# Optimization experiments

Measured on AMD Instinct MI355X. Metric: run time of the kernel, lower is better.

Reference implementation:

```python
import jax, jax.numpy as jnp
import numpy as np

B, T, M = 64, 32, 64
IN_DIM, GNN, H, L = 256, 256, 4, 3
TEMP, OUT, NH, NLT = 256, 512, 8, 2
DIST_THR = 0.3


def _ln(x, s, b, eps=1e-5):
    mu = jnp.mean(x, -1, keepdims=True)
    v = jnp.mean(jnp.square(x - mu), -1, keepdims=True)
    return (x - mu) * jax.lax.rsqrt(v + eps) * s + b


def setup_inputs() -> dict:
    key = jax.random.key(0)
    ks = iter(jax.random.split(key, 64))
    def nrm(shape, scale=0.05):
        return jax.random.normal(next(ks), shape, jnp.float32) * scale
    C = GNN // H
    return dict(
        drone_feats=jax.random.normal(next(ks), (B, T, M, IN_DIM), jnp.float32),
        boxes=jax.random.uniform(next(ks), (B, T, M, 5), jnp.float32),
        drone_mask=jnp.ones((B, T, M), jnp.float32),
        in_proj_W=nrm((GNN, IN_DIM)), in_proj_b=jnp.zeros((GNN,), jnp.float32),
        gat_lin_W=nrm((L, GNN, GNN)), gat_edge_W=nrm((L, 3, GNN)),
        gat_att_src=nrm((L, H, C)), gat_att_dst=nrm((L, H, C)), gat_att_edge=nrm((L, H, C)),
        gat_bias=jnp.zeros((L, GNN), jnp.float32),
        gat_ln_s=jnp.ones((L, GNN), jnp.float32), gat_ln_b=jnp.zeros((L, GNN), jnp.float32),
        temp_W=nrm((TEMP, GNN)), temp_b=jnp.zeros((TEMP,), jnp.float32),
        pos_emb=nrm((1, T, TEMP), 0.02),
        qkv_W=nrm((NLT, 3 * TEMP, TEMP)), qkv_b=jnp.zeros((NLT, 3 * TEMP), jnp.float32),
        attn_out_W=nrm((NLT, TEMP, TEMP)), attn_out_b=jnp.zeros((NLT, TEMP), jnp.float32),
        ln1_s=jnp.ones((NLT, TEMP), jnp.float32), ln1_b=jnp.zeros((NLT, TEMP), jnp.float32),
        ln2_s=jnp.ones((NLT, TEMP), jnp.float32), ln2_b=jnp.zeros((NLT, TEMP), jnp.float32),
        ff1_W=nrm((NLT, 2 * TEMP, TEMP)), ff1_b=jnp.zeros((NLT, 2 * TEMP), jnp.float32),
        ff2_W=nrm((NLT, TEMP, 2 * TEMP)), ff2_b=jnp.zeros((NLT, TEMP), jnp.float32),
        pool_W=nrm((1, TEMP)), pool_b=jnp.zeros((1,), jnp.float32),
        out_W=nrm((OUT, TEMP)), out_b=jnp.zeros((OUT,), jnp.float32),
        out_ln_s=jnp.ones((OUT,), jnp.float32), out_ln_b=jnp.zeros((OUT,), jnp.float32),
    )


def reference(drone_feats, boxes, drone_mask, in_proj_W, in_proj_b, gat_lin_W, gat_edge_W,
              gat_att_src, gat_att_dst, gat_att_edge, gat_bias, gat_ln_s, gat_ln_b,
              temp_W, temp_b, pos_emb, qkv_W, qkv_b, attn_out_W, attn_out_b,
              ln1_s, ln1_b, ln2_s, ln2_b, ff1_W, ff1_b, ff2_W, ff2_b,
              pool_W, pool_b, out_W, out_b, out_ln_s, out_ln_b):
    Bv, Tv, Mv, _ = drone_feats.shape
    Hh, Cc = gat_att_src.shape[1], gat_att_src.shape[2]
    valid = drone_mask > 0.5                                  # [B,T,M]

    # ---- batched radius-graph build (dense masked form over tiny M) ----
    pos = boxes[..., 1:3]                                     # [B,T,M,2]
    rel = pos[..., None, :, :] - pos[..., :, None, :]         # [B,T,s,d,2] = pos_d - pos_s
    sq = jnp.sum(jnp.square(rel), -1)
    dist = jnp.sqrt(jnp.maximum(sq, 1e-12))                   # [B,T,s,d]
    eye = jnp.eye(Mv, dtype=bool)
    pair_valid = valid[..., :, None] & valid[..., None, :]
    adj = pair_valid & (dist < DIST_THR) & (~eye)             # real directed edges (s->d)
    eattr = jnp.where(adj[..., None], jnp.concatenate([dist[..., None], rel], -1), 0.0)
    # GATConv(add_self_loops=True, fill_value='mean'): self-loop attr = mean incoming attr
    deg = jnp.maximum(jnp.sum(adj, axis=-2), 1).astype(eattr.dtype)   # incoming per dst
    loop_attr = jnp.sum(eattr, axis=-3) / deg[..., None]              # [B,T,M,3]
    eattr = jnp.where(eye[:, :, None], loop_attr[..., None, :, :], eattr)
    full_adj = adj | (eye & pair_valid)

    # ---- spatial GAT stack ----
    x = jnp.einsum('btmi,gi->btmg', drone_feats, in_proj_W) + in_proj_b
    x = x * valid[..., None]
    for l in range(gat_lin_W.shape[0]):
        h = jnp.einsum('btmg,gk->btmk', x, gat_lin_W[l]).reshape(Bv, Tv, Mv, Hh, Cc)
        a_src = jnp.einsum('btmhc,hc->btmh', h, gat_att_src[l])
        a_dst = jnp.einsum('btmhc,hc->btmh', h, gat_att_dst[l])
        w_e = jnp.einsum('ehc,hc->eh', gat_edge_W[l].reshape(3, Hh, Cc), gat_att_edge[l])
        a_edge = jnp.einsum('btsde,eh->btsdh', eattr, w_e)
        logits = a_src[..., :, None, :] + a_dst[..., None, :, :] + a_edge
        logits = jnp.where(logits >= 0, logits, 0.2 * logits)        # LeakyReLU(0.2)
        logits = jnp.where(full_adj[..., None], logits, jnp.float32(-1e9))
        alpha = jax.nn.softmax(logits, axis=-3)                      # softmax over src per dst
        msg = jnp.einsum('btsdh,btshc->btdhc', alpha, h).reshape(Bv, Tv, Mv, Hh * Cc) + gat_bias[l]
        x = jax.nn.relu(_ln(msg + x, gat_ln_s[l], gat_ln_b[l]))

    nvalid = jnp.maximum(jnp.sum(valid, -1), 1).astype(x.dtype)
    frame = jnp.sum(x * valid[..., None], axis=-2) / nvalid[..., None]   # [B,T,GNN]

    # ---- temporal transformer (norm_first, relu, 2 layers) ----
    y = jnp.einsum('btg,dg->btd', frame, temp_W) + temp_b
    y = y + pos_emb[:, :Tv, :]
    D = y.shape[-1]
    hd = D // NH
    for l in range(qkv_W.shape[0]):
        z = _ln(y, ln1_s[l], ln1_b[l])
        qkv = z @ qkv_W[l].T + qkv_b[l]
        q, k, v = jnp.split(qkv, 3, axis=-1)
        q = q.reshape(Bv, Tv, NH, hd).transpose(0, 2, 1, 3)
        k = k.reshape(Bv, Tv, NH, hd).transpose(0, 2, 1, 3)
        v = v.reshape(Bv, Tv, NH, hd).transpose(0, 2, 1, 3)
        att = jax.nn.softmax(jnp.einsum('bhqd,bhkd->bhqk', q, k) / jnp.sqrt(jnp.float32(hd)), -1)
        o = jnp.einsum('bhqk,bhkd->bhqd', att, v).transpose(0, 2, 1, 3).reshape(Bv, Tv, D)
        y = y + o @ attn_out_W[l].T + attn_out_b[l]
        z = _ln(y, ln2_s[l], ln2_b[l])
        y = y + jax.nn.relu(z @ ff1_W[l].T + ff1_b[l]) @ ff2_W[l].T + ff2_b[l]

    wts = jax.nn.softmax(y @ pool_W.T + pool_b, axis=1)   # [B,T,1]
    pooled = jnp.sum(y * wts, axis=1)                     # [B,D]
    out = pooled @ out_W.T + out_b
    return jax.nn.relu(_ln(out, out_ln_s, out_ln_b))
```

## Files before the change

### kernel.cpp

```cpp
#include <hip/hip_runtime.h>
#include <math.h>

#define BT 2048

typedef __attribute__((ext_vector_type(8))) short bf16x8;
typedef __attribute__((ext_vector_type(4))) float f32x4;
typedef __attribute__((ext_vector_type(4))) unsigned short u16x4;

__device__ inline unsigned short f2bf(float f) {
    union { float f; unsigned u; } v; v.f = f;
    unsigned r = (v.u >> 16) & 1u;
    return (unsigned short)((v.u + 0x7FFFu + r) >> 16);
}
__device__ inline float bf2f(unsigned short s) {
    union { unsigned u; float f; } v; v.u = ((unsigned)s) << 16;
    return v.f;
}

__device__ inline float dot4(const float4 a, const float4 b) {
    return fmaf(a.x, b.x, fmaf(a.y, b.y, fmaf(a.z, b.z, a.w * b.w)));
}

union F8 { float4 v2[2]; float f[8]; };

#define XP 264

__global__ __launch_bounds__(256) void k_prep(const float* __restrict__ inW,
                                              const float* __restrict__ gatW,
                                              unsigned short* __restrict__ dst) {
    int gid = blockIdx.x * 256 + threadIdx.x;
    int mat = gid >> 14;
    int r   = gid & 16383;
    int ks  = r >> 10;
    int nt  = (r >> 6) & 15;
    int lane = r & 63;
    int ln15 = lane & 15, q = lane >> 4;
    int n  = nt * 16 + ln15;
    int k0 = ks * 32 + q * 8;
    const float* src; bool tr;
    if (mat == 0) { src = inW; tr = true; }
    else          { src = gatW + (size_t)(mat - 1) * 65536; tr = false; }
    unsigned short* d = dst + ((size_t)mat * 16384 + r) * 16;
    if (ks < 8) {
        #pragma unroll
        for (int j = 0; j < 8; j++) {
            float v = tr ? src[n * 256 + k0 + j] : src[(size_t)(k0 + j) * 256 + n];
            unsigned short hi = f2bf(v);
            d[j]     = hi;
            d[8 + j] = f2bf(v - bf2f(hi));
        }
    } else {
        #pragma unroll
        for (int j = 0; j < 8; j++) { d[j] = 0; d[8 + j] = 0; }
    }
}

__global__ __launch_bounds__(512, 2) void k_gnn(const float* __restrict__ feats,
                                                const float* __restrict__ boxes,
                                                const float* __restrict__ maskp,
                                                const unsigned short* __restrict__ BswAll,
                                                const float* __restrict__ inb,
                                                const float* __restrict__ edgeW,
                                                const float* __restrict__ attSg,
                                                const float* __restrict__ attDg,
                                                const float* __restrict__ attEg,
                                                const float* __restrict__ gbias,
                                                const float* __restrict__ glns,
                                                const float* __restrict__ glnb,
                                                float* __restrict__ framebuf) {
    int bt = blockIdx.x;
    size_t fbase = (size_t)bt * 64 * 256;

    __shared__ unsigned short xH[64 * XP];
    __shared__ unsigned short xL[64 * XP];
    __shared__ unsigned short hT[256 * 136];
    __shared__ float pxS[64], pyS[64], vmS[64];
    __shared__ float loopS[192];
    __shared__ float asrcS[8][64], adstS[8][64];
    __shared__ float wESall[36];
    __shared__ float sumsS[64][8];
    __shared__ float mrsS[64][2];
    __shared__ float nvS;

    int tid = threadIdx.x, lane = tid & 63, w = tid >> 6;
    int ln15 = lane & 15, q = lane >> 4;
    int nt0 = w * 2;
    int head = w >> 1;
    int base_d = (w & 1) * 32;

    unsigned short* fH = hT;
    unsigned short* fL = hT + 64 * XP;

    if (tid < 64) {
        const float* bx = boxes + (size_t)(bt * 64 + tid) * 5;
        pxS[tid] = bx[1];
        pyS[tid] = bx[2];
        vmS[tid] = maskp[bt * 64 + tid];
    } else if (tid < 100) {
        int idx = tid - 64;
        int l = idx / 12, r2 = idx - l * 12;
        int e = r2 >> 2, h2 = r2 & 3;
        float sm = 0.f;
        const float* ew = edgeW + (size_t)l * 768 + e * 256 + h2 * 64;
        const float* ae = attEg + (size_t)l * 256 + h2 * 64;
        for (int c = 0; c < 64; c++) sm += ew[c] * ae[c];
        wESall[idx] = sm;
    }
    #pragma unroll
    for (int j = 0; j < 8; j++) {
        int g = j * 2048 + tid * 4;
        int row = g >> 8, col = g & 255;
        float4 v4 = *(const float4*)&feats[fbase + g];
        union { u16x4 v; unsigned short u[4]; } H4, L4;
        float vf[4] = {v4.x, v4.y, v4.z, v4.w};
        #pragma unroll
        for (int jj = 0; jj < 4; jj++) {
            H4.u[jj] = f2bf(vf[jj]);
            L4.u[jj] = f2bf(vf[jj] - bf2f(H4.u[jj]));
        }
        *(u16x4*)&fH[row * XP + col] = H4.v;
        *(u16x4*)&fL[row * XP + col] = L4.v;
    }
    __syncthreads();

    {
        int d = tid >> 3, part = tid & 7;
        float pxd = pxS[d], pyd = pyS[d];
        bool vd = vmS[d] > 0.5f;
        float deg = 0.f, s0 = 0.f, s1 = 0.f, s2 = 0.f;
        #pragma unroll
        for (int k = 0; k < 8; k++) {
            int s = part * 8 + k;
            float rx = pxd - pxS[s], ry = pyd - pyS[s];
            float dist = sqrtf(fmaxf(rx * rx + ry * ry, 1e-12f));
            bool adj = vd && (vmS[s] > 0.5f) && (dist < 0.3f) && (s != d);
            if (adj) { deg += 1.f; s0 += dist; s1 += rx; s2 += ry; }
        }
        #pragma unroll
        for (int off = 1; off < 8; off <<= 1) {
            deg += __shfl_xor(deg, off);
            s0  += __shfl_xor(s0, off);
            s1  += __shfl_xor(s1, off);
            s2  += __shfl_xor(s2, off);
        }
        if (part == 0) {
            float dg = fmaxf(deg, 1.f);
            loopS[d * 3 + 0] = s0 / dg;
            loopS[d * 3 + 1] = s1 / dg;
            loopS[d * 3 + 2] = s2 / dg;
        }
    }
    if (tid == 0) {
        float nv = 0.f;
        for (int m = 0; m < 64; m++) nv += vmS[m] > 0.5f ? 1.f : 0.f;
        nvS = fmaxf(nv, 1.f);
    }

    {
        f32x4 acc[4][2];
        #pragma unroll
        for (int mt = 0; mt < 4; mt++)
            #pragma unroll
            for (int ntl = 0; ntl < 2; ntl++) acc[mt][ntl] = (f32x4){0.f, 0.f, 0.f, 0.f};
        for (int ks = 0; ks < 8; ks++) {
            bf16x8 bhi[2], blo[2];
            #pragma unroll
            for (int ntl = 0; ntl < 2; ntl++) {
                const unsigned short* fb = &BswAll[((size_t)(ks * 16 + nt0 + ntl) * 64 + lane) * 16];
                bhi[ntl] = *(const bf16x8*)&fb[0];
                blo[ntl] = *(const bf16x8*)&fb[8];
            }
            #pragma unroll
            for (int mt = 0; mt < 4; mt++) {
                int ao = (mt * 16 + ln15) * XP + ks * 32 + q * 8;
                bf16x8 ahi = *(const bf16x8*)&fH[ao];
                bf16x8 alo = *(const bf16x8*)&fL[ao];
                #pragma unroll
                for (int ntl = 0; ntl < 2; ntl++) {
                    acc[mt][ntl] = __builtin_amdgcn_mfma_f32_16x16x32_bf16(ahi, bhi[ntl], acc[mt][ntl], 0, 0, 0);
                    acc[mt][ntl] = __builtin_amdgcn_mfma_f32_16x16x32_bf16(alo, bhi[ntl], acc[mt][ntl], 0, 0, 0);
                    acc[mt][ntl] = __builtin_amdgcn_mfma_f32_16x16x32_bf16(ahi, blo[ntl], acc[mt][ntl], 0, 0, 0);
                }
            }
        }
        #pragma unroll
        for (int ntl = 0; ntl < 2; ntl++) {
            int c = (nt0 + ntl) * 16 + ln15;
            float bv = inb[c];
            #pragma unroll
            for (int mt = 0; mt < 4; mt++) {
                #pragma unroll
                for (int r = 0; r < 4; r++) {
                    int m = mt * 16 + q * 4 + r;
                    float v = (acc[mt][ntl][r] + bv) * (vmS[m] > 0.5f ? 1.f : 0.f);
                    unsigned short hi = f2bf(v);
                    xH[m * XP + c] = hi;
                    xL[m * XP + c] = f2bf(v - bf2f(hi));
                }
            }
        }
    }
    __syncthreads();

    for (int l = 0; l < 3; l++) {
        const unsigned short* BswL = BswAll + (size_t)(1 + l) * 16384 * 16;
        const float* attSl = attSg + (size_t)l * 256;
        const float* attDl = attDg + (size_t)l * 256;
        const float* biasl = gbias + (size_t)l * 256;
        const float* lnsl  = glns + (size_t)l * 256;
        const float* lnbl  = glnb + (size_t)l * 256;
        const float* wES   = wESall + l * 12;

        f32x4 acc[4][2];
        #pragma unroll
        for (int mt = 0; mt < 4; mt++)
            #pragma unroll
            for (int ntl = 0; ntl < 2; ntl++) acc[mt][ntl] = (f32x4){0.f, 0.f, 0.f, 0.f};
        for (int ks = 0; ks < 8; ks++) {
            bf16x8 bhi[2], blo[2];
            #pragma unroll
            for (int ntl = 0; ntl < 2; ntl++) {
                const unsigned short* fb = &BswL[((size_t)(ks * 16 + nt0 + ntl) * 64 + lane) * 16];
                bhi[ntl] = *(const bf16x8*)&fb[0];
                blo[ntl] = *(const bf16x8*)&fb[8];
            }
            #pragma unroll
            for (int mt = 0; mt < 4; mt++) {
                int ao = (mt * 16 + ln15) * XP + ks * 32 + q * 8;
                bf16x8 ahi = *(const bf16x8*)&xH[ao];
                bf16x8 alo = *(const bf16x8*)&xL[ao];
                #pragma unroll
                for (int ntl = 0; ntl < 2; ntl++) {
                    acc[mt][ntl] = __builtin_amdgcn_mfma_f32_16x16x32_bf16(ahi, bhi[ntl], acc[mt][ntl], 0, 0, 0);
                    acc[mt][ntl] = __builtin_amdgcn_mfma_f32_16x16x32_bf16(alo, bhi[ntl], acc[mt][ntl], 0, 0, 0);
                    acc[mt][ntl] = __builtin_amdgcn_mfma_f32_16x16x32_bf16(ahi, blo[ntl], acc[mt][ntl], 0, 0, 0);
                }
            }
        }

        {
            float pSrc[4][4], pDst[4][4];
            #pragma unroll
            for (int mt = 0; mt < 4; mt++)
                #pragma unroll
                for (int r = 0; r < 4; r++) { pSrc[mt][r] = 0.f; pDst[mt][r] = 0.f; }
            #pragma unroll
            for (int ntl = 0; ntl < 2; ntl++) {
                int c = (nt0 + ntl) * 16 + ln15;
                float aS = attSl[c], aD = attDl[c];
                #pragma unroll
                for (int mt = 0; mt < 4; mt++) {
                    #pragma unroll
                    for (int r = 0; r < 4; r++) {
                        float v = acc[mt][ntl][r];
                        pSrc[mt][r] = fmaf(v, aS, pSrc[mt][r]);
                        pDst[mt][r] = fmaf(v, aD, pDst[mt][r]);
                        unsigned short hi = f2bf(v);
                        unsigned short lo = f2bf(v - bf2f(hi));
                        int s = mt * 16 + q * 4 + r;
                        hT[c * 136 + s] = hi;
                        hT[c * 136 + 64 + s] = lo;
                    }
                }
            }
            #pragma unroll
            for (int off = 1; off < 16; off <<= 1) {
                #pragma unroll
                for (int mt = 0; mt < 4; mt++)
                    #pragma unroll
                    for (int r = 0; r < 4; r++) {
                        pSrc[mt][r] += __shfl_xor(pSrc[mt][r], off);
                        pDst[mt][r] += __shfl_xor(pDst[mt][r], off);
                    }
            }
            if (ln15 == 0) {
                #pragma unroll
                for (int mt = 0; mt < 4; mt++)
                    #pragma unroll
                    for (int r = 0; r < 4; r++) {
                        int m = mt * 16 + q * 4 + r;
                        asrcS[w][m] = pSrc[mt][r];
                        adstS[w][m] = pDst[mt][r];
                    }
            }
        }
        __syncthreads();

        f32x4 macc[2][4];
        #pragma unroll
        for (int t = 0; t < 2; t++)
            #pragma unroll
            for (int ct = 0; ct < 4; ct++) macc[t][ct] = (f32x4){0.f, 0.f, 0.f, 0.f};
        {
            float pxd[2], pyd[2], adstv[2], lp0[2], lp1[2], lp2[2];
            int dcur[2];
            bool vdv[2];
            #pragma unroll
            for (int t = 0; t < 2; t++) {
                int d = base_d + t * 16 + ln15;
                dcur[t] = d;
                pxd[t] = pxS[d]; pyd[t] = pyS[d];
                vdv[t] = vmS[d] > 0.5f;
                adstv[t] = adstS[2 * head][d] + adstS[2 * head + 1][d];
                lp0[t] = loopS[d * 3 + 0];
                lp1[t] = loopS[d * 3 + 1];
                lp2[t] = loopS[d * 3 + 2];
            }
            float we0 = wES[head], we1 = wES[4 + head], we2 = wES[8 + head];

            float lg[2][16];
            #pragma unroll
            for (int ks = 0; ks < 2; ks++) {
                int s0 = ks * 32 + q * 8;
                F8 PX, PY, VM, AS, A1;
                PX.v2[0] = *(const float4*)&pxS[s0]; PX.v2[1] = *(const float4*)&pxS[s0 + 4];
                PY.v2[0] = *(const float4*)&pyS[s0]; PY.v2[1] = *(const float4*)&pyS[s0 + 4];
                VM.v2[0] = *(const float4*)&vmS[s0]; VM.v2[1] = *(const float4*)&vmS[s0 + 4];
                AS.v2[0] = *(const float4*)&asrcS[2 * head][s0];
                AS.v2[1] = *(const float4*)&asrcS[2 * head][s0 + 4];
                A1.v2[0] = *(const float4*)&asrcS[2 * head + 1][s0];
                A1.v2[1] = *(const float4*)&asrcS[2 * head + 1][s0 + 4];
                #pragma unroll
                for (int j = 0; j < 8; j++) {
                    int s = s0 + j;
                    float vsf = VM.f[j];
                    float asv = AS.f[j] + A1.f[j];
                    #pragma unroll
                    for (int t = 0; t < 2; t++) {
                        float rx = pxd[t] - PX.f[j], ry = pyd[t] - PY.f[j];
                        float dist = sqrtf(fmaxf(rx * rx + ry * ry, 1e-12f));
                        bool self = (s == dcur[t]);
                        bool adj = vdv[t] && (vsf > 0.5f) && (dist < 0.3f) && !self;
                        float e0 = adj ? dist : (self ? lp0[t] : 0.f);
                        float e1 = adj ? rx   : (self ? lp1[t] : 0.f);
                        float e2 = adj ? ry   : (self ? lp2[t] : 0.f);
                        bool fa = adj || (self && vdv[t]);
                        float lv = asv + adstv[t] + e0 * we0 + e1 * we1 + e2 * we2;
                        lv = lv >= 0.f ? lv : 0.2f * lv;
                        lg[t][ks * 8 + j] = fa ? lv : -1e9f;
                    }
                }
            }

            bf16x8 ah[2][2], al[2][2];
            #pragma unroll
            for (int t = 0; t < 2; t++) {
                float mx = lg[t][0];
                #pragma unroll
                for (int j = 1; j < 16; j++) mx = fmaxf(mx, lg[t][j]);
                mx = fmaxf(mx, __shfl_xor(mx, 16));
                mx = fmaxf(mx, __shfl_xor(mx, 32));
                float ee[16], sm = 0.f;
                #pragma unroll
                for (int j = 0; j < 16; j++) { ee[j] = __expf(lg[t][j] - mx); sm += ee[j]; }
                sm += __shfl_xor(sm, 16);
                sm += __shfl_xor(sm, 32);
                float inv = 1.f / sm;
                #pragma unroll
                for (int ks2 = 0; ks2 < 2; ks2++) {
                    union { bf16x8 v; unsigned short u[8]; } H, L;
                    #pragma unroll
                    for (int j = 0; j < 8; j++) {
                        float a = ee[ks2 * 8 + j] * inv;
                        unsigned short hi = f2bf(a);
                        H.u[j] = hi;
                        L.u[j] = f2bf(a - bf2f(hi));
                    }
                    ah[t][ks2] = H.v; al[t][ks2] = L.v;
                }
            }

            #pragma unroll
            for (int t = 0; t < 2; t++) {
                #pragma unroll
                for (int ks2 = 0; ks2 < 2; ks2++) {
                    #pragma unroll
                    for (int ct = 0; ct < 4; ct++) {
                        const unsigned short* hb =
                            &hT[(size_t)(head * 64 + ct * 16 + ln15) * 136 + ks2 * 32 + q * 8];
                        bf16x8 bhi = *(const bf16x8*)&hb[0];
                        bf16x8 blo = *(const bf16x8*)&hb[64];
                        macc[t][ct] = __builtin_amdgcn_mfma_f32_16x16x32_bf16(ah[t][ks2], bhi, macc[t][ct], 0, 0, 0);
                        macc[t][ct] = __builtin_amdgcn_mfma_f32_16x16x32_bf16(al[t][ks2], bhi, macc[t][ct], 0, 0, 0);
                        macc[t][ct] = __builtin_amdgcn_mfma_f32_16x16x32_bf16(ah[t][ks2], blo, macc[t][ct], 0, 0, 0);
                    }
                }
            }
        }

        {
            float bsv[4], scv[4], bbv[4];
            #pragma unroll
            for (int ct = 0; ct < 4; ct++) {
                int c = head * 64 + ct * 16 + ln15;
                bsv[ct] = biasl[c];
                scv[ct] = lnsl[c];
                bbv[ct] = lnbl[c];
            }
            float xo[2][4][4];
            #pragma unroll
            for (int t = 0; t < 2; t++)
                #pragma unroll
                for (int r = 0; r < 4; r++) {
                    int d = base_d + t * 16 + q * 4 + r;
                    #pragma unroll
                    for (int ct = 0; ct < 4; ct++) {
                        int o = d * XP + head * 64 + ct * 16 + ln15;
                        xo[t][ct][r] = bf2f(xH[o]) + bf2f(xL[o]);
                    }
                }
            float ps[8], ps2[8];
            #pragma unroll
            for (int t = 0; t < 2; t++)
                #pragma unroll
                for (int r = 0; r < 4; r++) {
                    float s = 0.f, s2 = 0.f;
                    #pragma unroll
                    for (int ct = 0; ct < 4; ct++) {
                        float v = macc[t][ct][r] + xo[t][ct][r] + bsv[ct];
                        s += v; s2 += v * v;
                    }
                    ps[t * 4 + r] = s; ps2[t * 4 + r] = s2;
                }
            #pragma unroll
            for (int off = 1; off < 16; off <<= 1) {
                #pragma unroll
                for (int i = 0; i < 8; i++) {
                    ps[i]  += __shfl_xor(ps[i], off);
                    ps2[i] += __shfl_xor(ps2[i], off);
                }
            }
            if (ln15 == 0) {
                #pragma unroll
                for (int t = 0; t < 2; t++)
                    #pragma unroll
                    for (int r = 0; r < 4; r++) {
                        int d = base_d + t * 16 + q * 4 + r;
                        sumsS[d][head * 2 + 0] = ps[t * 4 + r];
                        sumsS[d][head * 2 + 1] = ps2[t * 4 + r];
                    }
            }
            __syncthreads();
            if (tid < 64) {
                float S  = sumsS[tid][0] + sumsS[tid][2] + sumsS[tid][4] + sumsS[tid][6];
                float S2 = sumsS[tid][1] + sumsS[tid][3] + sumsS[tid][5] + sumsS[tid][7];
                float mu = S * (1.f / 256.f);
                float var = S2 * (1.f / 256.f) - mu * mu;
                mrsS[tid][0] = mu;
                mrsS[tid][1] = rsqrtf(var + 1e-5f);
            }
            __syncthreads();
            #pragma unroll
            for (int t = 0; t < 2; t++)
                #pragma unroll
                for (int r = 0; r < 4; r++) {
                    int d = base_d + t * 16 + q * 4 + r;
                    float mu = mrsS[d][0], rs = mrsS[d][1];
                    #pragma unroll
                    for (int ct = 0; ct < 4; ct++) {
                        float v = (macc[t][ct][r] + xo[t][ct][r] + bsv[ct] - mu) * rs * scv[ct] + bbv[ct];
                        v = fmaxf(v, 0.f);
                        unsigned short hi = f2bf(v);
                        int o = d * XP + head * 64 + ct * 16 + ln15;
                        xH[o] = hi;
                        xL[o] = f2bf(v - bf2f(hi));
                    }
                }
        }
        __syncthreads();
    }

    if (tid < 256) {
        float s = 0.f;
        for (int m = 0; m < 64; m++) {
            float xv = bf2f(xH[m * XP + tid]) + bf2f(xL[m * XP + tid]);
            s += xv * (vmS[m] > 0.5f ? 1.f : 0.f);
        }
        framebuf[(size_t)bt * 256 + tid] = s / nvS;
    }
}

__global__ __launch_bounds__(256) void k_temp4(const float* __restrict__ framebuf,
                                               const float* __restrict__ tW,
                                               const float* __restrict__ tb,
                                               const float* __restrict__ pe,
                                               float* __restrict__ ybuf) {
    int b4 = blockIdx.x;
    int tid = threadIdx.x;
    __shared__ float frS[4][256];
    #pragma unroll
    for (int t = 0; t < 4; t++) frS[t][tid] = framebuf[(size_t)(b4 * 4 + t) * 256 + tid];
    __syncthreads();
    float acc[4];
    #pragma unroll
    for (int t = 0; t < 4; t++) acc[t] = tb[tid] + pe[((b4 * 4 + t) & 31) * 256 + tid];
    const float* wrow = tW + (size_t)tid * 256;
    for (int g = 0; g < 256; g += 4) {
        float4 wv = *(const float4*)&wrow[g];
        #pragma unroll
        for (int t = 0; t < 4; t++) acc[t] += dot4(*(const float4*)&frS[t][g], wv);
    }
    #pragma unroll
    for (int t = 0; t < 4; t++) ybuf[(size_t)(b4 * 4 + t) * 256 + tid] = acc[t];
}

__global__ __launch_bounds__(256) void k_ln_qkv4(const float* __restrict__ ybuf,
                                                 const float* __restrict__ ln_s,
                                                 const float* __restrict__ ln_b,
                                                 const float* __restrict__ qW,
                                                 const float* __restrict__ qb,
                                                 float* __restrict__ qkvbuf) {
    int b4 = blockIdx.x, tid = threadIdx.x;
    int lane = tid & 63, wv = tid >> 6;
    __shared__ float zS[4][256];
    {
        int bt = b4 * 4 + wv;
        float4 yv = *(const float4*)&ybuf[(size_t)bt * 256 + lane * 4];
        float s = yv.x + yv.y + yv.z + yv.w;
        float s2 = yv.x * yv.x + yv.y * yv.y + yv.z * yv.z + yv.w * yv.w;
        #pragma unroll
        for (int off = 1; off < 64; off <<= 1) { s += __shfl_xor(s, off); s2 += __shfl_xor(s2, off); }
        float mu = s * (1.f / 256.f);
        float var = s2 * (1.f / 256.f) - mu * mu;
        float rstd = rsqrtf(var + 1e-5f);
        float4 ls = *(const float4*)&ln_s[lane * 4];
        float4 lb = *(const float4*)&ln_b[lane * 4];
        float4 z;
        z.x = (yv.x - mu) * rstd * ls.x + lb.x;
        z.y = (yv.y - mu) * rstd * ls.y + lb.y;
        z.z = (yv.z - mu) * rstd * ls.z + lb.z;
        z.w = (yv.w - mu) * rstd * ls.w + lb.w;
        *(float4*)&zS[wv][lane * 4] = z;
    }
    __syncthreads();
    for (int r = 0; r < 3; r++) {
        int j = r * 256 + tid;
        float acc[4];
        float bv = qb[j];
        #pragma unroll
        for (int t = 0; t < 4; t++) acc[t] = bv;
        const float* wrow = qW + (size_t)j * 256;
        for (int i = 0; i < 256; i += 4) {
            float4 wv4 = *(const float4*)&wrow[i];
            #pragma unroll
            for (int t = 0; t < 4; t++) acc[t] += dot4(*(const float4*)&zS[t][i], wv4);
        }
        #pragma unroll
        for (int t = 0; t < 4; t++) qkvbuf[(size_t)(b4 * 4 + t) * 768 + j] = acc[t];
    }
}

__global__ __launch_bounds__(64) void k_attn(const float* __restrict__ qkvbuf,
                                             float* __restrict__ obuf) {
    int blk = blockIdx.x;
    int b = blk >> 3, h = blk & 7;
    int tid = threadIdx.x;
    __shared__ float Ks[32 * 32], Vs[32 * 32];
    for (int idx = tid; idx < 1024; idx += 64) {
        int tk = idx >> 5, c = idx & 31;
        size_t qbase = ((size_t)(b * 32 + tk)) * 768 + h * 32 + c;
        Ks[idx] = qkvbuf[qbase + 256];
        Vs[idx] = qkvbuf[qbase + 512];
    }
    __syncthreads();
    if (tid < 32) {
        int tq = tid;
        float qv[32];
        size_t qb0 = ((size_t)(b * 32 + tq)) * 768 + h * 32;
        #pragma unroll
        for (int c = 0; c < 32; c++) qv[c] = qkvbuf[qb0 + c];
        float scr[32];
        float mx = -1e30f;
        #pragma unroll
        for (int tk = 0; tk < 32; tk++) {
            float dd = 0.f;
            #pragma unroll
            for (int c = 0; c < 32; c++) dd = fmaf(qv[c], Ks[tk * 32 + c], dd);
            dd *= 0.17677669529663687f;
            scr[tk] = dd;
            mx = fmaxf(mx, dd);
        }
        float sm = 0.f;
        #pragma unroll
        for (int tk = 0; tk < 32; tk++) { scr[tk] = __expf(scr[tk] - mx); sm += scr[tk]; }
        float inv = 1.f / sm;
        float o[32];
        #pragma unroll
        for (int c = 0; c < 32; c++) o[c] = 0.f;
        #pragma unroll
        for (int tk = 0; tk < 32; tk++) {
            float a = scr[tk] * inv;
            #pragma unroll
            for (int c = 0; c < 32; c++) o[c] = fmaf(a, Vs[tk * 32 + c], o[c]);
        }
        size_t ob = ((size_t)(b * 32 + tq)) * 256 + h * 32;
        #pragma unroll
        for (int c = 0; c < 32; c++) obuf[ob + c] = o[c];
    }
}

__global__ __launch_bounds__(256) void k_attn_out4(const float* __restrict__ obuf,
                                                   const float* __restrict__ W,
                                                   const float* __restrict__ bvec,
                                                   float* __restrict__ ybuf) {
    int b4 = blockIdx.x, tid = threadIdx.x;
    int lane = tid & 63, wv = tid >> 6;
    __shared__ float oS[4][256];
    *(float4*)&oS[wv][lane * 4] = *(const float4*)&obuf[(size_t)(b4 * 4 + wv) * 256 + lane * 4];
    __syncthreads();
    float acc[4];
    float bv = bvec[tid];
    #pragma unroll
    for (int t = 0; t < 4; t++) acc[t] = bv;
    const float* wrow = W + (size_t)tid * 256;
    for (int i = 0; i < 256; i += 4) {
        float4 wv4 = *(const float4*)&wrow[i];
        #pragma unroll
        for (int t = 0; t < 4; t++) acc[t] += dot4(*(const float4*)&oS[t][i], wv4);
    }
    #pragma unroll
    for (int t = 0; t < 4; t++) ybuf[(size_t)(b4 * 4 + t) * 256 + tid] += acc[t];
}

__global__ __launch_bounds__(256) void k_ff4(float* __restrict__ ybuf,
                                             const float* __restrict__ ln_s,
                                             const float* __restrict__ ln_b,
                                             const float* __restrict__ W1,
                                             const float* __restrict__ b1,
                                             const float* __restrict__ W2,
                                             const float* __restrict__ b2) {
    int b4 = blockIdx.x, tid = threadIdx.x;
    int lane = tid & 63, wv = tid >> 6;
    __shared__ float zS[4][256];
    __shared__ float fS[4][512];
    {
        int bt = b4 * 4 + wv;
        float4 yv = *(const float4*)&ybuf[(size_t)bt * 256 + lane * 4];
        float s = yv.x + yv.y + yv.z + yv.w;
        float s2 = yv.x * yv.x + yv.y * yv.y + yv.z * yv.z + yv.w * yv.w;
        #pragma unroll
        for (int off = 1; off < 64; off <<= 1) { s += __shfl_xor(s, off); s2 += __shfl_xor(s2, off); }
        float mu = s * (1.f / 256.f);
        float var = s2 * (1.f / 256.f) - mu * mu;
        float rstd = rsqrtf(var + 1e-5f);
        float4 ls = *(const float4*)&ln_s[lane * 4];
        float4 lb = *(const float4*)&ln_b[lane * 4];
        float4 z;
        z.x = (yv.x - mu) * rstd * ls.x + lb.x;
        z.y = (yv.y - mu) * rstd * ls.y + lb.y;
        z.z = (yv.z - mu) * rstd * ls.z + lb.z;
        z.w = (yv.w - mu) * rstd * ls.w + lb.w;
        *(float4*)&zS[wv][lane * 4] = z;
    }
    __syncthreads();
    for (int r = 0; r < 2; r++) {
        int j = r * 256 + tid;
        float acc[4];
        float bv = b1[j];
        #pragma unroll
        for (int t = 0; t < 4; t++) acc[t] = bv;
        const float* wrow = W1 + (size_t)j * 256;
        for (int i = 0; i < 256; i += 4) {
            float4 wv4 = *(const float4*)&wrow[i];
            #pragma unroll
            for (int t = 0; t < 4; t++) acc[t] += dot4(*(const float4*)&zS[t][i], wv4);
        }
        #pragma unroll
        for (int t = 0; t < 4; t++) fS[t][j] = fmaxf(acc[t], 0.f);
    }
    __syncthreads();
    float acc[4];
    float bv = b2[tid];
    #pragma unroll
    for (int t = 0; t < 4; t++) acc[t] = bv;
    const float* wrow = W2 + (size_t)tid * 512;
    for (int jj = 0; jj < 512; jj += 4) {
        float4 wv4 = *(const float4*)&wrow[jj];
        #pragma unroll
        for (int t = 0; t < 4; t++) acc[t] += dot4(*(const float4*)&fS[t][jj], wv4);
    }
    #pragma unroll
    for (int t = 0; t < 4; t++) {
        size_t idx = (size_t)(b4 * 4 + t) * 256 + tid;
        ybuf[idx] = ybuf[idx] + acc[t];
    }
}

__global__ __launch_bounds__(256) void k_pool_out(const float* __restrict__ ybuf,
                                                  const float* __restrict__ pW,
                                                  const float* __restrict__ pb,
                                                  const float* __restrict__ oW,
                                                  const float* __restrict__ ob,
                                                  const float* __restrict__ lns,
                                                  const float* __restrict__ lnb,
                                                  float* __restrict__ dout) {
    int b = blockIdx.x, tid = threadIdx.x;
    __shared__ float redP[256];
    __shared__ float wS[32];
    __shared__ float pS[256];
    __shared__ float red[8];
    int tq = tid >> 3, part = tid & 7;
    float partial = 0.f;
    {
        const float* yrow = ybuf + ((size_t)(b * 32 + tq)) * 256 + part * 32;
        const float* pwp = pW + part * 32;
        #pragma unroll
        for (int j = 0; j < 32; j += 4) {
            float4 yv = *(const float4*)&yrow[j];
            float4 wv = *(const float4*)&pwp[j];
            partial += dot4(yv, wv);
        }
    }
    redP[tid] = partial;
    __syncthreads();
    if (tid < 32) {
        float s = pb[0];
        for (int p = 0; p < 8; p++) s += redP[tid * 8 + p];
        float mx = s;
        #pragma unroll
        for (int off = 16; off; off >>= 1) mx = fmaxf(mx, __shfl_xor(mx, off));
        float e = __expf(s - mx);
        float sm = e;
        #pragma unroll
        for (int off = 16; off; off >>= 1) sm += __shfl_xor(sm, off);
        wS[tid] = e / sm;
    }
    __syncthreads();
    float p = 0.f;
    for (int t = 0; t < 32; t++) p += ybuf[((size_t)(b * 32 + t)) * 256 + tid] * wS[t];
    pS[tid] = p;
    __syncthreads();
    float accs[2];
    for (int r = 0; r < 2; r++) {
        int j = r * 256 + tid;
        float acc = ob[j];
        const float* wrow = oW + (size_t)j * 256;
        for (int g = 0; g < 256; g += 4) {
            float4 pv = *(const float4*)&pS[g];
            float4 wv = *(const float4*)&wrow[g];
            acc += dot4(pv, wv);
        }
        accs[r] = acc;
    }
    float s = accs[0] + accs[1];
    float s2 = accs[0] * accs[0] + accs[1] * accs[1];
    #pragma unroll
    for (int off = 32; off; off >>= 1) {
        s += __shfl_xor(s, off);
        s2 += __shfl_xor(s2, off);
    }
    int wid = threadIdx.x >> 6;
    int lane = threadIdx.x & 63;
    if (lane == 0) { red[wid] = s; red[4 + wid] = s2; }
    __syncthreads();
    s = red[0] + red[1] + red[2] + red[3];
    s2 = red[4] + red[5] + red[6] + red[7];
    float mu = s * (1.f / 512.f);
    float var = s2 * (1.f / 512.f) - mu * mu;
    float rstd = rsqrtf(var + 1e-5f);
    dout[b * 512 + tid]       = fmaxf((accs[0] - mu) * rstd * lns[tid] + lnb[tid], 0.f);
    dout[b * 512 + tid + 256] = fmaxf((accs[1] - mu) * rstd * lns[tid + 256] + lnb[tid + 256], 0.f);
}

extern "C" void kernel_launch(void* const* d_in, const int* in_sizes, int n_in,
                              void* d_out, int out_size, void* d_ws, size_t ws_size,
                              hipStream_t stream) {
    const float* drone_feats = (const float*)d_in[0];
    const float* boxes       = (const float*)d_in[1];
    const float* drone_mask  = (const float*)d_in[2];
    const float* in_proj_W   = (const float*)d_in[3];
    const float* in_proj_b   = (const float*)d_in[4];
    const float* gat_lin_W   = (const float*)d_in[5];
    const float* gat_edge_W  = (const float*)d_in[6];
    const float* gat_att_src = (const float*)d_in[7];
    const float* gat_att_dst = (const float*)d_in[8];
    const float* gat_att_edge= (const float*)d_in[9];
    const float* gat_bias    = (const float*)d_in[10];
    const float* gat_ln_s    = (const float*)d_in[11];
    const float* gat_ln_b    = (const float*)d_in[12];
    const float* temp_W      = (const float*)d_in[13];
    const float* temp_b      = (const float*)d_in[14];
    const float* pos_emb     = (const float*)d_in[15];
    const float* qkv_W       = (const float*)d_in[16];
    const float* qkv_b       = (const float*)d_in[17];
    const float* attn_out_W  = (const float*)d_in[18];
    const float* attn_out_b  = (const float*)d_in[19];
    const float* ln1_s       = (const float*)d_in[20];
    const float* ln1_b       = (const float*)d_in[21];
    const float* ln2_s       = (const float*)d_in[22];
    const float* ln2_b       = (const float*)d_in[23];
    const float* ff1_W       = (const float*)d_in[24];
    const float* ff1_b       = (const float*)d_in[25];
    const float* ff2_W       = (const float*)d_in[26];
    const float* ff2_b       = (const float*)d_in[27];
    const float* pool_W      = (const float*)d_in[28];
    const float* pool_b      = (const float*)d_in[29];
    const float* out_W       = (const float*)d_in[30];
    const float* out_b       = (const float*)d_in[31];
    const float* out_ln_s    = (const float*)d_in[32];
    const float* out_ln_b    = (const float*)d_in[33];
    float* out = (float*)d_out;

    float* ws = (float*)d_ws;
    unsigned short* Bsw = (unsigned short*)ws;
    size_t off = (size_t)(4 * 16384 * 16) / 2;
    float* framebuf = ws + off; off += (size_t)BT * 256;
    float* ybuf   = ws + off; off += (size_t)BT * 256;
    float* qkvbuf = ws + off; off += (size_t)BT * 768;
    float* obuf   = ws + off; off += (size_t)BT * 256;

    k_prep<<<dim3(256), dim3(256), 0, stream>>>(in_proj_W, gat_lin_W, Bsw);
    k_gnn<<<dim3(BT), dim3(512), 0, stream>>>(drone_feats, boxes, drone_mask, Bsw,
        in_proj_b, gat_edge_W, gat_att_src, gat_att_dst, gat_att_edge,
        gat_bias, gat_ln_s, gat_ln_b, framebuf);
    k_temp4<<<dim3(BT / 4), dim3(256), 0, stream>>>(framebuf, temp_W, temp_b, pos_emb, ybuf);
    for (int l = 0; l < 2; l++) {
        k_ln_qkv4<<<dim3(BT / 4), dim3(256), 0, stream>>>(ybuf, ln1_s + l * 256, ln1_b + l * 256,
            qkv_W + (size_t)l * 768 * 256, qkv_b + l * 768, qkvbuf);
        k_attn<<<dim3(512), dim3(64), 0, stream>>>(qkvbuf, obuf);
        k_attn_out4<<<dim3(BT / 4), dim3(256), 0, stream>>>(obuf,
            attn_out_W + (size_t)l * 65536, attn_out_b + l * 256, ybuf);
        k_ff4<<<dim3(BT / 4), dim3(256), 0, stream>>>(ybuf, ln2_s + l * 256, ln2_b + l * 256,
            ff1_W + (size_t)l * 131072, ff1_b + l * 512,
            ff2_W + (size_t)l * 131072, ff2_b + l * 256);
    }
    k_pool_out<<<dim3(64), dim3(256), 0, stream>>>(ybuf, pool_W, pool_b, out_W, out_b,
                                                   out_ln_s, out_ln_b, out);
}
```

Baseline: 1.136 ms.

## Alias GNN shared buffers and preload residual into accumulators to raise occupancy

Merges the xH/xL and hT shared arrays into one union buffer, which adds barriers where the regions are reused. The residual plus bias is loaded into the attention accumulators before the aggregation MFMAs, so the separate xo register array goes away. The softmax/aggregation loop now handles one tile at a time to cut live registers, and launch bounds ask for 4 blocks per CU instead of 2. The aim is lower LDS and VGPR use for higher occupancy, at the cost of extra syncs and possible spills if the register budget is too tight.

```diff
diff --git a/kernel.cpp b/kernel.cpp
--- a/kernel.cpp
+++ b/kernel.cpp
@@ -55,7 +55,7 @@
     }
 }
 
-__global__ __launch_bounds__(512, 2) void k_gnn(const float* __restrict__ feats,
+__global__ __launch_bounds__(512, 4) void k_gnn(const float* __restrict__ feats,
                                                 const float* __restrict__ boxes,
                                                 const float* __restrict__ maskp,
                                                 const unsigned short* __restrict__ BswAll,
@@ -71,9 +71,7 @@
     int bt = blockIdx.x;
     size_t fbase = (size_t)bt * 64 * 256;
 
-    __shared__ unsigned short xH[64 * XP];
-    __shared__ unsigned short xL[64 * XP];
-    __shared__ unsigned short hT[256 * 136];
+    __shared__ unsigned short U[256 * 136];
     __shared__ float pxS[64], pyS[64], vmS[64];
     __shared__ float loopS[192];
     __shared__ float asrcS[8][64], adstS[8][64];
@@ -88,8 +86,8 @@
     int head = w >> 1;
     int base_d = (w & 1) * 32;
 
-    unsigned short* fH = hT;
-    unsigned short* fL = hT + 64 * XP;
+    unsigned short* xH = U;
+    unsigned short* xL = U + 64 * XP;
 
     if (tid < 64) {
         const float* bx = boxes + (size_t)(bt * 64 + tid) * 5;
@@ -118,8 +116,8 @@
             H4.u[jj] = f2bf(vf[jj]);
             L4.u[jj] = f2bf(vf[jj] - bf2f(H4.u[jj]));
         }
-        *(u16x4*)&fH[row * XP + col] = H4.v;
-        *(u16x4*)&fL[row * XP + col] = L4.v;
+        *(u16x4*)&xH[row * XP + col] = H4.v;
+        *(u16x4*)&xL[row * XP + col] = L4.v;
     }
     __syncthreads();
 
@@ -173,8 +171,8 @@
             #pragma unroll
             for (int mt = 0; mt < 4; mt++) {
                 int ao = (mt * 16 + ln15) * XP + ks * 32 + q * 8;
-                bf16x8 ahi = *(const bf16x8*)&fH[ao];
-                bf16x8 alo = *(const bf16x8*)&fL[ao];
+                bf16x8 ahi = *(const bf16x8*)&xH[ao];
+                bf16x8 alo = *(const bf16x8*)&xL[ao];
                 #pragma unroll
                 for (int ntl = 0; ntl < 2; ntl++) {
                     acc[mt][ntl] = __builtin_amdgcn_mfma_f32_16x16x32_bf16(ahi, bhi[ntl], acc[mt][ntl], 0, 0, 0);
@@ -183,6 +181,7 @@
                 }
             }
         }
+        __syncthreads();
         #pragma unroll
         for (int ntl = 0; ntl < 2; ntl++) {
             int c = (nt0 + ntl) * 16 + ln15;
@@ -238,6 +237,25 @@
             }
         }
 
+        f32x4 macc[2][4];
+        {
+            #pragma unroll
+            for (int ct = 0; ct < 4; ct++) {
+                int c = head * 64 + ct * 16 + ln15;
+                float bv = biasl[c];
+                #pragma unroll
+                for (int t = 0; t < 2; t++) {
+                    #pragma unroll
+                    for (int r = 0; r < 4; r++) {
+                        int d = base_d + t * 16 + q * 4 + r;
+                        int o = d * XP + c;
+                        macc[t][ct][r] = bf2f(xH[o]) + bf2f(xL[o]) + bv;
+                    }
+                }
+            }
+        }
+        __syncthreads();
+
         {
             float pSrc[4][4], pDst[4][4];
             #pragma unroll
@@ -258,8 +276,8 @@
                         unsigned short hi = f2bf(v);
                         unsigned short lo = f2bf(v - bf2f(hi));
                         int s = mt * 16 + q * 4 + r;
-                        hT[c * 136 + s] = hi;
-                        hT[c * 136 + 64 + s] = lo;
+                        U[c * 136 + s] = hi;
+                        U[c * 136 + 64 + s] = lo;
                     }
                 }
             }
@@ -286,129 +304,99 @@
         }
         __syncthreads();
 
-        f32x4 macc[2][4];
-        #pragma unroll
-        for (int t = 0; t < 2; t++)
-            #pragma unroll
-            for (int ct = 0; ct < 4; ct++) macc[t][ct] = (f32x4){0.f, 0.f, 0.f, 0.f};
         {
-            float pxd[2], pyd[2], adstv[2], lp0[2], lp1[2], lp2[2];
-            int dcur[2];
-            bool vdv[2];
+            float we0 = wES[head], we1 = wES[4 + head], we2 = wES[8 + head];
             #pragma unroll
             for (int t = 0; t < 2; t++) {
                 int d = base_d + t * 16 + ln15;
-                dcur[t] = d;
-                pxd[t] = pxS[d]; pyd[t] = pyS[d];
-                vdv[t] = vmS[d] > 0.5f;
-                adstv[t] = adstS[2 * head][d] + adstS[2 * head + 1][d];
-                lp0[t] = loopS[d * 3 + 0];
-                lp1[t] = loopS[d * 3 + 1];
-                lp2[t] = loopS[d * 3 + 2];
-            }
-            float we0 = wES[head], we1 = wES[4 + head], we2 = wES[8 + head];
-
-            float lg[2][16];
-            #pragma unroll
-            for (int ks = 0; ks < 2; ks++) {
-                int s0 = ks * 32 + q * 8;
-                F8 PX, PY, VM, AS, A1;
-                PX.v2[0] = *(const float4*)&pxS[s0]; PX.v2[1] = *(const float4*)&pxS[s0 + 4];
-                PY.v2[0] = *(const float4*)&pyS[s0]; PY.v2[1] = *(const float4*)&pyS[s0 + 4];
-                VM.v2[0] = *(const float4*)&vmS[s0]; VM.v2[1] = *(const float4*)&vmS[s0 + 4];
-                AS.v2[0] = *(const float4*)&asrcS[2 * head][s0];
-                AS.v2[1] = *(const float4*)&asrcS[2 * head][s0 + 4];
-                A1.v2[0] = *(const float4*)&asrcS[2 * head + 1][s0];
-                A1.v2[1] = *(const float4*)&asrcS[2 * head + 1][s0 + 4];
-                #pragma unroll
-                for (int j = 0; j < 8; j++) {
-                    int s = s0 + j;
-                    float vsf = VM.f[j];
-                    float asv = AS.f[j] + A1.f[j];
-                    #pragma unroll
-                    for (int t = 0; t < 2; t++) {
-                        float rx = pxd[t] - PX.f[j], ry = pyd[t] - PY.f[j];
+                float pxd = pxS[d], pyd = pyS[d];
+                bool vdv = vmS[d] > 0.5f;
+                float adstv = adstS[2 * head][d] + adstS[2 * head + 1][d];
+                float lp0 = loopS[d * 3 + 0];
+                float lp1 = loopS[d * 3 + 1];
+                float lp2 = loopS[d * 3 + 2];
+
+                float lg[16];
+                #pragma unroll
+                for (int ks = 0; ks < 2; ks++) {
+                    int s0 = ks * 32 + q * 8;
+                    F8 PX, PY, VM, AS, A1;
+                    PX.v2[0] = *(const float4*)&pxS[s0]; PX.v2[1] = *(const float4*)&pxS[s0 + 4];
+                    PY.v2[0] = *(const float4*)&pyS[s0]; PY.v2[1] = *(const float4*)&pyS[s0 + 4];
+                    VM.v2[0] = *(const float4*)&vmS[s0]; VM.v2[1] = *(const float4*)&vmS[s0 + 4];
+                    AS.v2[0] = *(const float4*)&asrcS[2 * head][s0];
+                    AS.v2[1] = *(const float4*)&asrcS[2 * head][s0 + 4];
+                    A1.v2[0] = *(const float4*)&asrcS[2 * head + 1][s0];
+                    A1.v2[1] = *(const float4*)&asrcS[2 * head + 1][s0 + 4];
+                    #pragma unroll
+                    for (int j = 0; j < 8; j++) {
+                        int s = s0 + j;
+                        float vsf = VM.f[j];
+                        float asv = AS.f[j] + A1.f[j];
+                        float rx = pxd - PX.f[j], ry = pyd - PY.f[j];
                         float dist = sqrtf(fmaxf(rx * rx + ry * ry, 1e-12f));
-                        bool self = (s == dcur[t]);
-                        bool adj = vdv[t] && (vsf > 0.5f) && (dist < 0.3f) && !self;
-                        float e0 = adj ? dist : (self ? lp0[t] : 0.f);
-                        float e1 = adj ? rx   : (self ? lp1[t] : 0.f);
-                        float e2 = adj ? ry   : (self ? lp2[t] : 0.f);
-                        bool fa = adj || (self && vdv[t]);
-                        float lv = asv + adstv[t] + e0 * we0 + e1 * we1 + e2 * we2;
+                        bool self = (s == d);
+                        bool adj = vdv && (vsf > 0.5f) && (dist < 0.3f) && !self;
+                        float e0 = adj ? dist : (self ? lp0 : 0.f);
+                        float e1 = adj ? rx   : (self ? lp1 : 0.f);
+                        float e2 = adj ? ry   : (self ? lp2 : 0.f);
+                        bool fa = adj || (self && vdv);
+                        float lv = asv + adstv + e0 * we0 + e1 * we1 + e2 * we2;
                         lv = lv >= 0.f ? lv : 0.2f * lv;
-                        lg[t][ks * 8 + j] = fa ? lv : -1e9f;
-                    }
-                }
-            }
-
-            bf16x8 ah[2][2], al[2][2];
-            #pragma unroll
-            for (int t = 0; t < 2; t++) {
-                float mx = lg[t][0];
-                #pragma unroll
-                for (int j = 1; j < 16; j++) mx = fmaxf(mx, lg[t][j]);
+                        lg[ks * 8 + j] = fa ? lv : -1e9f;
+                    }
+                }
+
+                float mx = lg[0];
+                #pragma unroll
+                for (int j = 1; j < 16; j++) mx = fmaxf(mx, lg[j]);
                 mx = fmaxf(mx, __shfl_xor(mx, 16));
                 mx = fmaxf(mx, __shfl_xor(mx, 32));
-                float ee[16], sm = 0.f;
-                #pragma unroll
-                for (int j = 0; j < 16; j++) { ee[j] = __expf(lg[t][j] - mx); sm += ee[j]; }
+                float sm = 0.f;
+                #pragma unroll
+                for (int j = 0; j < 16; j++) { lg[j] = __expf(lg[j] - mx); sm += lg[j]; }
                 sm += __shfl_xor(sm, 16);
                 sm += __shfl_xor(sm, 32);
                 float inv = 1.f / sm;
+
+                bf16x8 ah[2], al[2];
                 #pragma unroll
                 for (int ks2 = 0; ks2 < 2; ks2++) {
                     union { bf16x8 v; unsigned short u[8]; } H, L;
                     #pragma unroll
                     for (int j = 0; j < 8; j++) {
-                        float a = ee[ks2 * 8 + j] * inv;
+                        float a = lg[ks2 * 8 + j] * inv;
                         unsigned short hi = f2bf(a);
                         H.u[j] = hi;
                         L.u[j] = f2bf(a - bf2f(hi));
                     }
-                    ah[t][ks2] = H.v; al[t][ks2] = L.v;
-                }
-            }
-
-            #pragma unroll
-            for (int t = 0; t < 2; t++) {
+                    ah[ks2] = H.v; al[ks2] = L.v;
+                }
+
                 #pragma unroll
                 for (int ks2 = 0; ks2 < 2; ks2++) {
                     #pragma unroll
                     for (int ct = 0; ct < 4; ct++) {
                         const unsigned short* hb =
-                            &hT[(size_t)(head * 64 + ct * 16 + ln15) * 136 + ks2 * 32 + q * 8];
+                            &U[(size_t)(head * 64 + ct * 16 + ln15) * 136 + ks2 * 32 + q * 8];
                         bf16x8 bhi = *(const bf16x8*)&hb[0];
                         bf16x8 blo = *(const bf16x8*)&hb[64];
-                        macc[t][ct] = __builtin_amdgcn_mfma_f32_16x16x32_bf16(ah[t][ks2], bhi, macc[t][ct], 0, 0, 0);
-                        macc[t][ct] = __builtin_amdgcn_mfma_f32_16x16x32_bf16(al[t][ks2], bhi, macc[t][ct], 0, 0, 0);
-                        macc[t][ct] = __builtin_amdgcn_mfma_f32_16x16x32_bf16(ah[t][ks2], blo, macc[t][ct], 0, 0, 0);
+                        macc[t][ct] = __builtin_amdgcn_mfma_f32_16x16x32_bf16(ah[ks2], bhi, macc[t][ct], 0, 0, 0);
+                        macc[t][ct] = __builtin_amdgcn_mfma_f32_16x16x32_bf16(al[ks2], bhi, macc[t][ct], 0, 0, 0);
+                        macc[t][ct] = __builtin_amdgcn_mfma_f32_16x16x32_bf16(ah[ks2], blo, macc[t][ct], 0, 0, 0);
                     }
                 }
             }
         }
 
         {
-            float bsv[4], scv[4], bbv[4];
+            float scv[4], bbv[4];
             #pragma unroll
             for (int ct = 0; ct < 4; ct++) {
                 int c = head * 64 + ct * 16 + ln15;
-                bsv[ct] = biasl[c];
                 scv[ct] = lnsl[c];
                 bbv[ct] = lnbl[c];
             }
-            float xo[2][4][4];
-            #pragma unroll
-            for (int t = 0; t < 2; t++)
-                #pragma unroll
-                for (int r = 0; r < 4; r++) {
-                    int d = base_d + t * 16 + q * 4 + r;
-                    #pragma unroll
-                    for (int ct = 0; ct < 4; ct++) {
-                        int o = d * XP + head * 64 + ct * 16 + ln15;
-                        xo[t][ct][r] = bf2f(xH[o]) + bf2f(xL[o]);
-                    }
-                }
             float ps[8], ps2[8];
             #pragma unroll
             for (int t = 0; t < 2; t++)
@@ -417,7 +405,7 @@
                     float s = 0.f, s2 = 0.f;
                     #pragma unroll
                     for (int ct = 0; ct < 4; ct++) {
-                        float v = macc[t][ct][r] + xo[t][ct][r] + bsv[ct];
+                        float v = macc[t][ct][r];
                         s += v; s2 += v * v;
                     }
                     ps[t * 4 + r] = s; ps2[t * 4 + r] = s2;
@@ -458,7 +446,7 @@
                     float mu = mrsS[d][0], rs = mrsS[d][1];
                     #pragma unroll
                     for (int ct = 0; ct < 4; ct++) {
-                        float v = (macc[t][ct][r] + xo[t][ct][r] + bsv[ct] - mu) * rs * scv[ct] + bbv[ct];
+                        float v = (macc[t][ct][r] - mu) * rs * scv[ct] + bbv[ct];
                         v = fmaxf(v, 0.f);
                         unsigned short hi = f2bf(v);
                         int o = d * XP + head * 64 + ct * 16 + ln15;
```

New measurement: 1.208 ms. +6.4%, slower.
